# Performance work log

Hardware: AMD Instinct MI355X
Metric: run time of the kernel (lower is better)

## Reference

```python
import jax, jax.numpy as jnp
import numpy as np

N = 256
MAX_LENGTH = 1024
BATCH = 32768


def _transition(n):
    # HiPPO-LegS transition matrices (float64 numpy, matches torch module)
    q = np.arange(n, dtype=np.float64)
    col, row = np.meshgrid(q, q)
    r = 2 * q + 1
    M = -(np.where(row >= col, r, 0) - np.diag(q))
    T = np.sqrt(np.diag(2 * q + 1))
    A = T @ M @ np.linalg.inv(T)
    B = np.diag(T)  # squeezed (N,)
    return A, B


def _build_stacked(n, max_length):
    # Bilinear (Tustin) discretization at every timescale t=1..max_length.
    A, B = _transition(n)
    ts = np.arange(1, max_length + 1, dtype=np.float64)  # (L,)
    At = A[None] / ts[:, None, None]                     # (L,N,N)
    Bt = B[None] / ts[:, None]                           # (L,N)
    I = np.eye(n)
    lhs = I[None] - At / 2                               # (L,N,N), lower triangular
    A_stacked = np.linalg.solve(lhs, I[None] + At / 2)   # (L,N,N)
    B_stacked = np.linalg.solve(lhs, Bt[..., None])[..., 0]  # (L,N)
    return A_stacked.astype(np.float32), B_stacked.astype(np.float32)


def setup_inputs() -> dict:
    key = jax.random.key(0)
    k1, k2 = jax.random.split(key)
    A_np, B_np = _build_stacked(N, MAX_LENGTH)
    return {
        "c": jax.random.normal(k1, (BATCH, N), dtype=jnp.float32),
        "f": jax.random.normal(k2, (BATCH, 1), dtype=jnp.float32),
        "A_stacked": jnp.asarray(A_np),  # (L, N, N) buffer
        "B_stacked": jnp.asarray(B_np),  # (L, N) buffer
        "t": 512,
    }


def reference(c, f, A_stacked, B_stacked, t):
    # F.linear(c, A) == c @ A.T ; then scaled add of new value f
    A = A_stacked[t]            # (N, N)
    b = B_stacked[t]            # (N,)
    return c @ A.T + b * f      # (BATCH, N)
```

## Files before the change

kernel.cpp:

```cpp
#include <hip/hip_runtime.h>
#include <cstdint>
#include <cstddef>

typedef _Float16 half8 __attribute__((ext_vector_type(8)));
typedef float f32x4 __attribute__((ext_vector_type(4)));

static constexpr int kN  = 256;
static constexpr int kBM = 64;
static constexpr size_t kHalfB  = 64 * 1024;
static constexpr size_t kLDS    = kHalfB;

__global__ __launch_bounds__(256) void hippo_prep(
    const float* __restrict__ A_stacked, const int* __restrict__ tptr,
    _Float16* __restrict__ a16)
{
    const int t = tptr[0];
    const float* __restrict__ A = A_stacked + (size_t)t * kN * kN;
    const int tid = blockIdx.x * 256 + threadIdx.x;
    const int ksh = tid >> 12;
    const int nt  = (tid >> 8) & 15;
    const int ks2 = (tid >> 6) & 3;
    const int l   = tid & 63;
    const int row = nt * 16 + (l & 15);
    const int k0  = (ksh * 4 + ks2) * 32 + ((l >> 4) << 3);
    const float* __restrict__ src = A + (size_t)row * kN + k0;
    f32x4 v0 = *(const f32x4*)(src);
    f32x4 v1 = *(const f32x4*)(src + 4);
    half8 h;
    h[0] = (_Float16)v0[0]; h[1] = (_Float16)v0[1];
    h[2] = (_Float16)v0[2]; h[3] = (_Float16)v0[3];
    h[4] = (_Float16)v1[0]; h[5] = (_Float16)v1[1];
    h[6] = (_Float16)v1[2]; h[7] = (_Float16)v1[3];
    ((half8*)a16)[tid] = h;
}

__global__ __launch_bounds__(256, 2) void hippo_gemm(
    const float* __restrict__ c, const float* __restrict__ f,
    const float* __restrict__ Bst, const int* __restrict__ tptr,
    const _Float16* __restrict__ a16, float* __restrict__ out)
{
    extern __shared__ char lds_raw[];

    const int tid  = threadIdx.x;
    const int l    = tid & 63;
    const int wid  = tid >> 6;
    const int lo16 = l & 15;
    const int hi4  = l >> 4;
    const int bid  = blockIdx.x;
    const int m0   = bid * kBM + wid * 16;
    const int hA   = bid & 1;
    const int hB   = hA ^ 1;

    const char* __restrict__ gsrcA = (const char*)a16 + (size_t)hA * kHalfB;
    #pragma unroll
    for (int i = 0; i < 16; ++i) {
        const size_t off = (size_t)(i * 4 + wid) * 1024 + (size_t)l * 16;
        __builtin_amdgcn_global_load_lds(
            (const __attribute__((address_space(1))) void*)(gsrcA + off),
            (__attribute__((address_space(3))) void*)(lds_raw + off),
            16, 0, 0);
    }

    const float* __restrict__ cptr = c + (size_t)(m0 + lo16) * kN + (hi4 << 3);
    f32x4 cv0[4], cv1[4];
    #pragma unroll
    for (int ks = 0; ks < 4; ++ks) {
        cv0[ks] = *(const f32x4*)(cptr + hA * 128 + ks * 32);
        cv1[ks] = *(const f32x4*)(cptr + hA * 128 + ks * 32 + 4);
    }

    const int t = tptr[0];
    const float* __restrict__ brow = Bst + (size_t)t * kN;
    float bvs[16];
    #pragma unroll
    for (int nt = 0; nt < 16; ++nt) bvs[nt] = brow[nt * 16 + lo16];
    float fv[4];
    #pragma unroll
    for (int r = 0; r < 4; ++r) fv[r] = f[m0 + (hi4 << 2) + r];

    __syncthreads();

    half8 af[4];
    #pragma unroll
    for (int ks = 0; ks < 4; ++ks) {
        af[ks][0] = (_Float16)cv0[ks][0]; af[ks][1] = (_Float16)cv0[ks][1];
        af[ks][2] = (_Float16)cv0[ks][2]; af[ks][3] = (_Float16)cv0[ks][3];
        af[ks][4] = (_Float16)cv1[ks][0]; af[ks][5] = (_Float16)cv1[ks][1];
        af[ks][6] = (_Float16)cv1[ks][2]; af[ks][7] = (_Float16)cv1[ks][3];
    }
    const half8* __restrict__ Bs = (const half8*)lds_raw;
    f32x4 acc[16];
    #pragma unroll
    for (int i = 0; i < 16; ++i) acc[i] = (f32x4){0.f, 0.f, 0.f, 0.f};
    #pragma unroll
    for (int ks = 0; ks < 4; ++ks) {
        #pragma unroll
        for (int nt = 0; nt < 16; ++nt) {
            half8 bf = Bs[(nt * 4 + ks) * 64 + l];
            acc[nt] = __builtin_amdgcn_mfma_f32_16x16x32_f16(af[ks], bf, acc[nt], 0, 0, 0);
        }
    }

    __syncthreads();

    const char* __restrict__ gsrcB = (const char*)a16 + (size_t)hB * kHalfB;
    #pragma unroll
    for (int i = 0; i < 16; ++i) {
        const size_t off = (size_t)(i * 4 + wid) * 1024 + (size_t)l * 16;
        __builtin_amdgcn_global_load_lds(
            (const __attribute__((address_space(1))) void*)(gsrcB + off),
            (__attribute__((address_space(3))) void*)(lds_raw + off),
            16, 0, 0);
    }
    f32x4 dv0[4], dv1[4];
    #pragma unroll
    for (int ks = 0; ks < 4; ++ks) {
        dv0[ks] = *(const f32x4*)(cptr + hB * 128 + ks * 32);
        dv1[ks] = *(const f32x4*)(cptr + hB * 128 + ks * 32 + 4);
    }

    __syncthreads();

    half8 ag[4];
    #pragma unroll
    for (int ks = 0; ks < 4; ++ks) {
        ag[ks][0] = (_Float16)dv0[ks][0]; ag[ks][1] = (_Float16)dv0[ks][1];
        ag[ks][2] = (_Float16)dv0[ks][2]; ag[ks][3] = (_Float16)dv0[ks][3];
        ag[ks][4] = (_Float16)dv1[ks][0]; ag[ks][5] = (_Float16)dv1[ks][1];
        ag[ks][6] = (_Float16)dv1[ks][2]; ag[ks][7] = (_Float16)dv1[ks][3];
    }
    #pragma unroll
    for (int ks = 0; ks < 4; ++ks) {
        #pragma unroll
        for (int nt = 0; nt < 16; ++nt) {
            half8 bf = Bs[(nt * 4 + ks) * 64 + l];
            acc[nt] = __builtin_amdgcn_mfma_f32_16x16x32_f16(ag[ks], bf, acc[nt], 0, 0, 0);
        }
    }

    float* __restrict__ obase = out + (size_t)(m0 + (hi4 << 2)) * kN + lo16;
    #pragma unroll
    for (int nt = 0; nt < 16; ++nt) {
        #pragma unroll
        for (int r = 0; r < 4; ++r)
            obase[(size_t)r * kN + nt * 16] = acc[nt][r] + bvs[nt] * fv[r];
    }
}

extern "C" void kernel_launch(void* const* d_in, const int* in_sizes, int n_in,
                              void* d_out, int out_size, void* d_ws, size_t ws_size,
                              hipStream_t stream) {
    const float* c   = (const float*)d_in[0];
    const float* f   = (const float*)d_in[1];
    const float* A   = (const float*)d_in[2];
    const float* B   = (const float*)d_in[3];
    const int*   t   = (const int*)d_in[4];
    float* out = (float*)d_out;
    _Float16* a16 = (_Float16*)d_ws;

    const int batch = in_sizes[0] / kN;

    hipFuncSetAttribute((const void*)hippo_gemm,
                        hipFuncAttributeMaxDynamicSharedMemorySize,
                        (int)kLDS);

    hipLaunchKernelGGL(hippo_prep, dim3(32), dim3(256), 0, stream, A, t, a16);
    hipLaunchKernelGGL(hippo_gemm, dim3(batch / kBM), dim3(256), kLDS, stream,
                       c, f, B, t, a16, out);
}
```

Measured before the change: 22.87 us.

## Fuse fp16 weight conversion into GEMM kernel, dropping the prep launch

Removes the separate prep kernel that converted A[t] to fp16 into a workspace. Each GEMM block now loads the fp32 A slice from global memory, converts it in registers and writes it to static LDS. The second-half c loads are hoisted ahead of the first MFMA loop. This saves a kernel launch and the workspace round trip. In exchange, every one of the 512 blocks reads 256KB of fp32 A instead of 128KB of fp16, and the asynchronous global-to-LDS loads become synchronous register loads.

```diff
diff --git a/kernel.cpp b/kernel.cpp
--- a/kernel.cpp
+++ b/kernel.cpp
@@ -7,39 +7,13 @@
 
 static constexpr int kN  = 256;
 static constexpr int kBM = 64;
-static constexpr size_t kHalfB  = 64 * 1024;
-static constexpr size_t kLDS    = kHalfB;
 
-__global__ __launch_bounds__(256) void hippo_prep(
-    const float* __restrict__ A_stacked, const int* __restrict__ tptr,
-    _Float16* __restrict__ a16)
+__global__ __launch_bounds__(256, 2) void hippo_fused(
+    const float* __restrict__ c, const float* __restrict__ f,
+    const float* __restrict__ A_stacked, const float* __restrict__ Bst,
+    const int* __restrict__ tptr, float* __restrict__ out)
 {
-    const int t = tptr[0];
-    const float* __restrict__ A = A_stacked + (size_t)t * kN * kN;
-    const int tid = blockIdx.x * 256 + threadIdx.x;
-    const int ksh = tid >> 12;
-    const int nt  = (tid >> 8) & 15;
-    const int ks2 = (tid >> 6) & 3;
-    const int l   = tid & 63;
-    const int row = nt * 16 + (l & 15);
-    const int k0  = (ksh * 4 + ks2) * 32 + ((l >> 4) << 3);
-    const float* __restrict__ src = A + (size_t)row * kN + k0;
-    f32x4 v0 = *(const f32x4*)(src);
-    f32x4 v1 = *(const f32x4*)(src + 4);
-    half8 h;
-    h[0] = (_Float16)v0[0]; h[1] = (_Float16)v0[1];
-    h[2] = (_Float16)v0[2]; h[3] = (_Float16)v0[3];
-    h[4] = (_Float16)v1[0]; h[5] = (_Float16)v1[1];
-    h[6] = (_Float16)v1[2]; h[7] = (_Float16)v1[3];
-    ((half8*)a16)[tid] = h;
-}
-
-__global__ __launch_bounds__(256, 2) void hippo_gemm(
-    const float* __restrict__ c, const float* __restrict__ f,
-    const float* __restrict__ Bst, const int* __restrict__ tptr,
-    const _Float16* __restrict__ a16, float* __restrict__ out)
-{
-    extern __shared__ char lds_raw[];
+    __shared__ _Float16 As[32768];
 
     const int tid  = threadIdx.x;
     const int l    = tid & 63;
@@ -50,15 +24,25 @@
     const int m0   = bid * kBM + wid * 16;
     const int hA   = bid & 1;
     const int hB   = hA ^ 1;
+    const int t    = tptr[0];
 
-    const char* __restrict__ gsrcA = (const char*)a16 + (size_t)hA * kHalfB;
+    const float* __restrict__ Abase = A_stacked + (size_t)t * kN * kN;
+
     #pragma unroll
     for (int i = 0; i < 16; ++i) {
-        const size_t off = (size_t)(i * 4 + wid) * 1024 + (size_t)l * 16;
-        __builtin_amdgcn_global_load_lds(
-            (const __attribute__((address_space(1))) void*)(gsrcA + off),
-            (__attribute__((address_space(3))) void*)(lds_raw + off),
-            16, 0, 0);
+        const int u   = i * 4 + wid;
+        const int nt  = u >> 2;
+        const int ks2 = u & 3;
+        const float* p = Abase + (size_t)(nt * 16 + lo16) * kN
+                         + (hA * 4 + ks2) * 32 + (hi4 << 3);
+        f32x4 v0 = *(const f32x4*)p;
+        f32x4 v1 = *(const f32x4*)(p + 4);
+        half8 h;
+        h[0] = (_Float16)v0[0]; h[1] = (_Float16)v0[1];
+        h[2] = (_Float16)v0[2]; h[3] = (_Float16)v0[3];
+        h[4] = (_Float16)v1[0]; h[5] = (_Float16)v1[1];
+        h[6] = (_Float16)v1[2]; h[7] = (_Float16)v1[3];
+        *(half8*)(As + (size_t)u * 512 + (size_t)l * 8) = h;
     }
 
     const float* __restrict__ cptr = c + (size_t)(m0 + lo16) * kN + (hi4 << 3);
@@ -69,7 +53,6 @@
         cv1[ks] = *(const f32x4*)(cptr + hA * 128 + ks * 32 + 4);
     }
 
-    const int t = tptr[0];
     const float* __restrict__ brow = Bst + (size_t)t * kN;
     float bvs[16];
     #pragma unroll
@@ -88,7 +71,14 @@
         af[ks][4] = (_Float16)cv1[ks][0]; af[ks][5] = (_Float16)cv1[ks][1];
         af[ks][6] = (_Float16)cv1[ks][2]; af[ks][7] = (_Float16)cv1[ks][3];
     }
-    const half8* __restrict__ Bs = (const half8*)lds_raw;
+    f32x4 dv0[4], dv1[4];
+    #pragma unroll
+    for (int ks = 0; ks < 4; ++ks) {
+        dv0[ks] = *(const f32x4*)(cptr + hB * 128 + ks * 32);
+        dv1[ks] = *(const f32x4*)(cptr + hB * 128 + ks * 32 + 4);
+    }
+
+    const half8* __restrict__ Bs = (const half8*)As;
     f32x4 acc[16];
     #pragma unroll
     for (int i = 0; i < 16; ++i) acc[i] = (f32x4){0.f, 0.f, 0.f, 0.f};
@@ -103,20 +93,21 @@
 
     __syncthreads();
 
-    const char* __restrict__ gsrcB = (const char*)a16 + (size_t)hB * kHalfB;
     #pragma unroll
     for (int i = 0; i < 16; ++i) {
-        const size_t off = (size_t)(i * 4 + wid) * 1024 + (size_t)l * 16;
-        __builtin_amdgcn_global_load_lds(
-            (const __attribute__((address_space(1))) void*)(gsrcB + off),
-            (__attribute__((address_space(3))) void*)(lds_raw + off),
-            16, 0, 0);
-    }
-    f32x4 dv0[4], dv1[4];
-    #pragma unroll
-    for (int ks = 0; ks < 4; ++ks) {
-        dv0[ks] = *(const f32x4*)(cptr + hB * 128 + ks * 32);
-        dv1[ks] = *(const f32x4*)(cptr + hB * 128 + ks * 32 + 4);
+        const int u   = i * 4 + wid;
+        const int nt  = u >> 2;
+        const int ks2 = u & 3;
+        const float* p = Abase + (size_t)(nt * 16 + lo16) * kN
+                         + (hB * 4 + ks2) * 32 + (hi4 << 3);
+        f32x4 v0 = *(const f32x4*)p;
+        f32x4 v1 = *(const f32x4*)(p + 4);
+        half8 h;
+        h[0] = (_Float16)v0[0]; h[1] = (_Float16)v0[1];
+        h[2] = (_Float16)v0[2]; h[3] = (_Float16)v0[3];
+        h[4] = (_Float16)v1[0]; h[5] = (_Float16)v1[1];
+        h[6] = (_Float16)v1[2]; h[7] = (_Float16)v1[3];
+        *(half8*)(As + (size_t)u * 512 + (size_t)l * 8) = h;
     }
 
     __syncthreads();
@@ -156,15 +147,9 @@
     const float* B   = (const float*)d_in[3];
     const int*   t   = (const int*)d_in[4];
     float* out = (float*)d_out;
-    _Float16* a16 = (_Float16*)d_ws;
 
     const int batch = in_sizes[0] / kN;
 
-    hipFuncSetAttribute((const void*)hippo_gemm,
-                        hipFuncAttributeMaxDynamicSharedMemorySize,
-                        (int)kLDS);
-
-    hipLaunchKernelGGL(hippo_prep, dim3(32), dim3(256), 0, stream, A, t, a16);
-    hipLaunchKernelGGL(hippo_gemm, dim3(batch / kBM), dim3(256), kLDS, stream,
-                       c, f, B, t, a16, out);
+    hipLaunchKernelGGL(hippo_fused, dim3(batch / kBM), dim3(256), 0, stream,
+                       c, f, A, B, t, out);
 }
```

Result: slower. 30.74 us (+34.5%).

## Switch to 32x32x16 MFMA with 2x2 warp tiling and earlier second-half prefetch

Applied to the files above, without the earlier changes.

Replaces the 16x16x32 MFMA tiles with 32x32x16 MFMA. Each wave now covers 32 rows and 128 columns in a 2x2 wave grid instead of 16 rows and all 256 columns. The prep kernel re-lays out the fp16 weight to match the new fragment order. The load of the second K-half of c is issued before the first MFMA loop, and the output stores are interleaved with the second-half MFMAs per column pair. The goals are fewer LDS B-fragment reads per FLOP, better MFMA efficiency, and overlapped epilogue stores, at the cost of more registers held live (dv arrays during the first loop).

```diff
diff --git a/kernel.cpp b/kernel.cpp
--- a/kernel.cpp
+++ b/kernel.cpp
@@ -3,12 +3,12 @@
 #include <cstddef>
 
 typedef _Float16 half8 __attribute__((ext_vector_type(8)));
-typedef float f32x4 __attribute__((ext_vector_type(4)));
+typedef float f32x4  __attribute__((ext_vector_type(4)));
+typedef float f32x16 __attribute__((ext_vector_type(16)));
 
-static constexpr int kN  = 256;
-static constexpr int kBM = 64;
-static constexpr size_t kHalfB  = 64 * 1024;
-static constexpr size_t kLDS    = kHalfB;
+static constexpr int kN = 256;
+static constexpr size_t kHalfB = 64 * 1024;
+static constexpr size_t kLDS   = kHalfB;
 
 __global__ __launch_bounds__(256) void hippo_prep(
     const float* __restrict__ A_stacked, const int* __restrict__ tptr,
@@ -17,12 +17,13 @@
     const int t = tptr[0];
     const float* __restrict__ A = A_stacked + (size_t)t * kN * kN;
     const int tid = blockIdx.x * 256 + threadIdx.x;
-    const int ksh = tid >> 12;
-    const int nt  = (tid >> 8) & 15;
-    const int ks2 = (tid >> 6) & 3;
+    const int u   = tid >> 6;
     const int l   = tid & 63;
-    const int row = nt * 16 + (l & 15);
-    const int k0  = (ksh * 4 + ks2) * 32 + ((l >> 4) << 3);
+    const int ksh = u >> 6;
+    const int nt  = (u >> 3) & 7;
+    const int kst = u & 7;
+    const int row = nt * 32 + (l & 31);
+    const int k0  = ksh * 128 + kst * 16 + ((l >> 5) << 3);
     const float* __restrict__ src = A + (size_t)row * kN + k0;
     f32x4 v0 = *(const f32x4*)(src);
     f32x4 v1 = *(const f32x4*)(src + 4);
@@ -44,10 +45,13 @@
     const int tid  = threadIdx.x;
     const int l    = tid & 63;
     const int wid  = tid >> 6;
-    const int lo16 = l & 15;
-    const int hi4  = l >> 4;
+    const int wm   = wid & 1;
+    const int wn   = wid >> 1;
+    const int lo32 = l & 31;
+    const int hi2  = l >> 5;
     const int bid  = blockIdx.x;
-    const int m0   = bid * kBM + wid * 16;
+    const int m0   = bid * 64 + wm * 32;
+    const int ntb  = wn * 4;
     const int hA   = bid & 1;
     const int hB   = hA ^ 1;
 
@@ -61,43 +65,54 @@
             16, 0, 0);
     }
 
-    const float* __restrict__ cptr = c + (size_t)(m0 + lo16) * kN + (hi4 << 3);
-    f32x4 cv0[4], cv1[4];
+    const float* __restrict__ cptr = c + (size_t)(m0 + lo32) * kN + (hi2 << 3);
+    f32x4 cv0[8], cv1[8];
     #pragma unroll
-    for (int ks = 0; ks < 4; ++ks) {
-        cv0[ks] = *(const f32x4*)(cptr + hA * 128 + ks * 32);
-        cv1[ks] = *(const f32x4*)(cptr + hA * 128 + ks * 32 + 4);
+    for (int kst = 0; kst < 8; ++kst) {
+        cv0[kst] = *(const f32x4*)(cptr + hA * 128 + kst * 16);
+        cv1[kst] = *(const f32x4*)(cptr + hA * 128 + kst * 16 + 4);
     }
 
     const int t = tptr[0];
-    const float* __restrict__ brow = Bst + (size_t)t * kN;
-    float bvs[16];
+    const float* __restrict__ brow = Bst + (size_t)t * kN + wn * 128;
+    float bvs[4];
     #pragma unroll
-    for (int nt = 0; nt < 16; ++nt) bvs[nt] = brow[nt * 16 + lo16];
-    float fv[4];
+    for (int nt = 0; nt < 4; ++nt) bvs[nt] = brow[nt * 32 + lo32];
+    float fv[16];
+    const float* __restrict__ fbase = f + m0 + (hi2 << 2);
     #pragma unroll
-    for (int r = 0; r < 4; ++r) fv[r] = f[m0 + (hi4 << 2) + r];
+    for (int r = 0; r < 16; ++r) fv[r] = fbase[(r & 3) + ((r >> 2) << 3)];
 
     __syncthreads();
 
-    half8 af[4];
+    half8 af[8];
     #pragma unroll
-    for (int ks = 0; ks < 4; ++ks) {
-        af[ks][0] = (_Float16)cv0[ks][0]; af[ks][1] = (_Float16)cv0[ks][1];
-        af[ks][2] = (_Float16)cv0[ks][2]; af[ks][3] = (_Float16)cv0[ks][3];
-        af[ks][4] = (_Float16)cv1[ks][0]; af[ks][5] = (_Float16)cv1[ks][1];
-        af[ks][6] = (_Float16)cv1[ks][2]; af[ks][7] = (_Float16)cv1[ks][3];
+    for (int kst = 0; kst < 8; ++kst) {
+        af[kst][0] = (_Float16)cv0[kst][0]; af[kst][1] = (_Float16)cv0[kst][1];
+        af[kst][2] = (_Float16)cv0[kst][2]; af[kst][3] = (_Float16)cv0[kst][3];
+        af[kst][4] = (_Float16)cv1[kst][0]; af[kst][5] = (_Float16)cv1[kst][1];
+        af[kst][6] = (_Float16)cv1[kst][2]; af[kst][7] = (_Float16)cv1[kst][3];
     }
+
+    f32x4 dv0[8], dv1[8];
+    #pragma unroll
+    for (int kst = 0; kst < 8; ++kst) {
+        dv0[kst] = *(const f32x4*)(cptr + hB * 128 + kst * 16);
+        dv1[kst] = *(const f32x4*)(cptr + hB * 128 + kst * 16 + 4);
+    }
+
     const half8* __restrict__ Bs = (const half8*)lds_raw;
-    f32x4 acc[16];
+    f32x16 acc[4];
     #pragma unroll
-    for (int i = 0; i < 16; ++i) acc[i] = (f32x4){0.f, 0.f, 0.f, 0.f};
+    for (int i = 0; i < 4; ++i)
+        #pragma unroll
+        for (int r = 0; r < 16; ++r) acc[i][r] = 0.f;
     #pragma unroll
-    for (int ks = 0; ks < 4; ++ks) {
+    for (int kst = 0; kst < 8; ++kst) {
         #pragma unroll
-        for (int nt = 0; nt < 16; ++nt) {
-            half8 bf = Bs[(nt * 4 + ks) * 64 + l];
-            acc[nt] = __builtin_amdgcn_mfma_f32_16x16x32_f16(af[ks], bf, acc[nt], 0, 0, 0);
+        for (int nt = 0; nt < 4; ++nt) {
+            half8 bf = Bs[((ntb + nt) * 8 + kst) * 64 + l];
+            acc[nt] = __builtin_amdgcn_mfma_f32_32x32x16_f16(af[kst], bf, acc[nt], 0, 0, 0);
         }
     }
 
@@ -112,38 +127,33 @@
             (__attribute__((address_space(3))) void*)(lds_raw + off),
             16, 0, 0);
     }
-    f32x4 dv0[4], dv1[4];
+    half8 ag[8];
     #pragma unroll
-    for (int ks = 0; ks < 4; ++ks) {
-        dv0[ks] = *(const f32x4*)(cptr + hB * 128 + ks * 32);
-        dv1[ks] = *(const f32x4*)(cptr + hB * 128 + ks * 32 + 4);
+    for (int kst = 0; kst < 8; ++kst) {
+        ag[kst][0] = (_Float16)dv0[kst][0]; ag[kst][1] = (_Float16)dv0[kst][1];
+        ag[kst][2] = (_Float16)dv0[kst][2]; ag[kst][3] = (_Float16)dv0[kst][3];
+        ag[kst][4] = (_Float16)dv1[kst][0]; ag[kst][5] = (_Float16)dv1[kst][1];
+        ag[kst][6] = (_Float16)dv1[kst][2]; ag[kst][7] = (_Float16)dv1[kst][3];
     }
 
     __syncthreads();
 
-    half8 ag[4];
+    float* __restrict__ obase = out + (size_t)(m0 + (hi2 << 2)) * kN + wn * 128 + lo32;
     #pragma unroll
-    for (int ks = 0; ks < 4; ++ks) {
-        ag[ks][0] = (_Float16)dv0[ks][0]; ag[ks][1] = (_Float16)dv0[ks][1];
-        ag[ks][2] = (_Float16)dv0[ks][2]; ag[ks][3] = (_Float16)dv0[ks][3];
-        ag[ks][4] = (_Float16)dv1[ks][0]; ag[ks][5] = (_Float16)dv1[ks][1];
-        ag[ks][6] = (_Float16)dv1[ks][2]; ag[ks][7] = (_Float16)dv1[ks][3];
-    }
-    #pragma unroll
-    for (int ks = 0; ks < 4; ++ks) {
+    for (int np = 0; np < 4; np += 2) {
         #pragma unroll
-        for (int nt = 0; nt < 16; ++nt) {
-            half8 bf = Bs[(nt * 4 + ks) * 64 + l];
-            acc[nt] = __builtin_amdgcn_mfma_f32_16x16x32_f16(ag[ks], bf, acc[nt], 0, 0, 0);
+        for (int kst = 0; kst < 8; ++kst) {
+            half8 bf0 = Bs[((ntb + np) * 8 + kst) * 64 + l];
+            half8 bf1 = Bs[((ntb + np + 1) * 8 + kst) * 64 + l];
+            acc[np]     = __builtin_amdgcn_mfma_f32_32x32x16_f16(ag[kst], bf0, acc[np], 0, 0, 0);
+            acc[np + 1] = __builtin_amdgcn_mfma_f32_32x32x16_f16(ag[kst], bf1, acc[np + 1], 0, 0, 0);
         }
-    }
-
-    float* __restrict__ obase = out + (size_t)(m0 + (hi4 << 2)) * kN + lo16;
-    #pragma unroll
-    for (int nt = 0; nt < 16; ++nt) {
         #pragma unroll
-        for (int r = 0; r < 4; ++r)
-            obase[(size_t)r * kN + nt * 16] = acc[nt][r] + bvs[nt] * fv[r];
+        for (int r = 0; r < 16; ++r) {
+            const int row_off = (r & 3) + ((r >> 2) << 3);
+            obase[(size_t)row_off * kN + np * 32]       = acc[np][r]     + bvs[np] * fv[r];
+            obase[(size_t)row_off * kN + (np + 1) * 32] = acc[np + 1][r] + bvs[np + 1] * fv[r];
+        }
     }
 }
 
@@ -165,6 +175,6 @@
                         (int)kLDS);
 
     hipLaunchKernelGGL(hippo_prep, dim3(32), dim3(256), 0, stream, A, t, a16);
-    hipLaunchKernelGGL(hippo_gemm, dim3(batch / kBM), dim3(256), kLDS, stream,
+    hipLaunchKernelGGL(hippo_gemm, dim3(batch / 64), dim3(256), kLDS, stream,
                        c, f, B, t, a16, out);
 }
```

New measurement: 26.43 us. 1.16x slower.
